# Optimization experiments

Measured on AMD Instinct MI355X. Metric: run time of the kernel, lower is better.

Reference implementation:

```python
import jax, jax.numpy as jnp
import numpy as np

NUM_CLASSES = 80
STRIDES = (8, 16, 32)
FEAT_HW = ((80, 80), (40, 40), (20, 20))
B = 32
MAX_GT = 60


def setup_inputs() -> dict:
    key = jax.random.key(0)
    ks = jax.random.split(key, 6)
    feats = {}
    for i, (s, (h, w)) in enumerate(zip(STRIDES, FEAT_HW)):
        feats[f"feat{s}"] = jax.random.normal(ks[i], (B, 5 + NUM_CLASSES, h, w), jnp.float32)
    u = jax.random.uniform(ks[3], (B, MAX_GT, 4), jnp.float32)
    # cx,cy in [0,640), w,h in [8,128): realistic pixel-space gt boxes for a 640x640 image
    gt_boxes = jnp.concatenate([u[..., :2] * 640.0, u[..., 2:] * 120.0 + 8.0], -1)
    gt_classes = jax.random.randint(ks[4], (B, MAX_GT), 0, NUM_CLASSES)
    num_gts = jax.random.randint(ks[5], (B,), 1, MAX_GT + 1)
    return dict(feat8=feats["feat8"], feat16=feats["feat16"], feat32=feats["feat32"],
                gt_boxes=gt_boxes, gt_classes=gt_classes, num_gts=num_gts)


def _decode(feat, stride):
    # torch get_output_and_grid: xy=(raw+grid)*stride, wh=exp(raw)*stride
    b, c, h, w = feat.shape
    yv, xv = jnp.meshgrid(jnp.arange(h), jnp.arange(w), indexing="ij")
    gx = xv.reshape(-1).astype(feat.dtype)  # [H*W]
    gy = yv.reshape(-1).astype(feat.dtype)
    out = feat.reshape(b, c, h * w).transpose(0, 2, 1)  # [B,A,C]
    xy = (out[..., :2] + jnp.stack([gx, gy], -1)[None]) * stride
    wh = jnp.exp(out[..., 2:4]) * stride
    return jnp.concatenate([xy, wh, out[..., 4:]], -1), gx, gy


def _pair_iou(a, b):
    # a: [G,4] xywh, b: [A,4] xywh -> [G,A] IoU (bboxes_iou, xyxy=False)
    tl = jnp.maximum(a[:, None, :2] - a[:, None, 2:] * 0.5, b[None, :, :2] - b[None, :, 2:] * 0.5)
    br = jnp.minimum(a[:, None, :2] + a[:, None, 2:] * 0.5, b[None, :, :2] + b[None, :, 2:] * 0.5)
    en = jnp.all(tl < br, -1)
    inter = jnp.where(en, jnp.prod(br - tl, -1), 0.0)
    area_a = jnp.prod(a[:, 2:], -1)
    area_b = jnp.prod(b[:, 2:], -1)
    return inter / (area_a[:, None] + area_b[None, :] - inter + 1e-16)


def _bce_logits(x, t):
    return jnp.maximum(x, 0.0) - x * t + jnp.log1p(jnp.exp(-jnp.abs(x)))


def _iou_loss(pred, tgt):
    # IOUloss(loss_type='iou'): 1 - iou^2, per box
    tl = jnp.maximum(pred[..., :2] - pred[..., 2:] * 0.5, tgt[..., :2] - tgt[..., 2:] * 0.5)
    br = jnp.minimum(pred[..., :2] + pred[..., 2:] * 0.5, tgt[..., :2] + tgt[..., 2:] * 0.5)
    en = jnp.all(tl < br, -1)
    inter = jnp.where(en, jnp.prod(br - tl, -1), 0.0)
    union = jnp.prod(pred[..., 2:], -1) + jnp.prod(tgt[..., 2:], -1) - inter
    iou = inter / (union + 1e-16)
    return 1.0 - iou ** 2


def _assign(boxes, cls_lo, obj_lo, gtb, gtc, vmask, cx, cy, st):
    # SimOTA per image. boxes [A,4], cls_lo [A,C], obj_lo [A], gtb [G,4], gtc [G] int,
    # vmask [G] bool (gt padding), cx/cy/st [A] anchor centers & strides.
    G, A = gtb.shape[0], boxes.shape[0]
    iou = _pair_iou(gtb, boxes)  # [G,A]
    gx, gy = gtb[:, :1], gtb[:, 1:2]
    gw, gh = gtb[:, 2:3], gtb[:, 3:4]
    in_box = ((cx[None] > gx - 0.5 * gw) & (cx[None] < gx + 0.5 * gw) &
              (cy[None] > gy - 0.5 * gh) & (cy[None] < gy + 0.5 * gh))
    R = 2.5  # center sampling radius (in strides)
    in_ctr = ((cx[None] > gx - R * st[None]) & (cx[None] < gx + R * st[None]) &
              (cy[None] > gy - R * st[None]) & (cy[None] < gy + R * st[None]))
    fg = ((in_box | in_ctr) & vmask[:, None]).any(0)  # [A] candidate anchors
    in_both = (in_box & in_ctr).astype(boxes.dtype)
    # pairwise cls cost: BCE(sqrt(sig(cls)*sig(obj)), onehot(gt_cls)).sum(-1),
    # decomposed to avoid the [G,A,C] tensor: sum_c bce0 + (bce1-bce0)[gt_cls]
    p = jnp.clip(jnp.sqrt(jax.nn.sigmoid(cls_lo) * jax.nn.sigmoid(obj_lo)[:, None]), 1e-7, 1.0 - 1e-7)
    bce1 = -jnp.log(p)          # [A,C]
    bce0 = -jnp.log(1.0 - p)    # [A,C]
    cls_cost = bce0.sum(-1)[None, :] + (bce1 - bce0)[:, gtc].T  # [G,A]
    cost = (cls_cost + 3.0 * (-jnp.log(iou + 1e-8))
            + 100000.0 * (1.0 - in_both)
            + 1e9 * (~fg)[None, :].astype(boxes.dtype)
            + 1e9 * (~vmask)[:, None].astype(boxes.dtype))
    K = 10  # n_candidate_k
    topk_ious, _ = jax.lax.top_k(iou * fg[None, :], K)
    dyn_k = jnp.maximum(topk_ious.sum(-1).astype(jnp.int32), 1)  # clamp(int(sum), min=1)
    _, pos = jax.lax.top_k(-cost, K)  # [G,K] lowest-cost anchors per gt
    sel = (jnp.arange(K)[None, :] < dyn_k[:, None]).astype(boxes.dtype)
    matching = jnp.zeros((G, A), boxes.dtype).at[jnp.arange(G)[:, None], pos].set(sel)
    matching = matching * vmask[:, None].astype(boxes.dtype)
    # resolve anchors claimed by >1 gt: keep min-cost gt
    conflict = matching.sum(0) > 1
    best_gt = jnp.argmin(cost, axis=0)  # [A]
    matching = jnp.where(conflict[None, :], jax.nn.one_hot(best_gt, G, dtype=matching.dtype).T, matching)
    fg_final = matching.sum(0) > 0  # [A]
    matched = jnp.argmax(matching, axis=0)  # [A]
    pred_iou = (matching * iou).sum(0)  # [A]
    cls_t = jax.nn.one_hot(gtc[matched], NUM_CLASSES, dtype=boxes.dtype) * pred_iou[:, None]
    reg_t = gtb[matched]
    return fg_final, cls_t, reg_t


def _forward(feat8, feat16, feat32, gt_boxes, gt_classes, num_gts):
    outs, cxs, cys, sts = [], [], [], []
    for f, s in zip((feat8, feat16, feat32), STRIDES):
        o, gx, gy = _decode(f, float(s))
        outs.append(o)
        cxs.append((gx + 0.5) * s)
        cys.append((gy + 0.5) * s)
        sts.append(jnp.full_like(gx, s))
    preds = jnp.concatenate(outs, 1)  # [B,A,5+C]
    cx = jnp.concatenate(cxs)
    cy = jnp.concatenate(cys)
    st = jnp.concatenate(sts)
    boxes = preds[..., :4]
    obj_lo = preds[..., 4]
    cls_lo = preds[..., 5:]
    vmask = jnp.arange(MAX_GT)[None, :] < num_gts[:, None]
    fg, cls_t, reg_t = jax.vmap(_assign, in_axes=(0, 0, 0, 0, 0, 0, None, None, None))(
        boxes, cls_lo, obj_lo, gt_boxes, gt_classes, vmask, cx, cy, st)
    # SimOTA assignment is no_grad in YOLOX: targets are constants wrt preds
    fg = jax.lax.stop_gradient(fg)
    cls_t = jax.lax.stop_gradient(cls_t)
    reg_t = jax.lax.stop_gradient(reg_t)
    fg_f = fg.astype(boxes.dtype)
    num_fg = jnp.maximum(fg_f.sum(), 1.0)
    loss_iou = (_iou_loss(boxes, reg_t) * fg_f).sum()
    loss_obj = _bce_logits(obj_lo, fg_f * 0.9).sum()  # obj_targets * 0.9 smoothing
    loss_cls = (_bce_logits(cls_lo, cls_t) * fg_f[..., None]).sum()
    REG_WEIGHT = 5.0
    return (REG_WEIGHT * loss_iou + loss_obj + loss_cls) / num_fg


def reference(feat8, feat16, feat32, gt_boxes, gt_classes, num_gts):
    return _forward(feat8, feat16, feat32, gt_boxes, gt_classes, num_gts)
```

## Files before the change

kernel.cpp:

```cpp
#include <hip/hip_runtime.h>

constexpr int kB = 32;
constexpr int kA = 8400;
constexpr int kG = 60;
constexpr int kC = 80;
constexpr int kK = 10;
constexpr int kNBx = (kA + 255)/256;
constexpr int kNB = kNBx * kB;

__device__ __forceinline__ float fexp(float x){ return __expf(x); }
__device__ __forceinline__ float flog(float x){ return __logf(x); }
__device__ __forceinline__ float frcp(float x){ return __builtin_amdgcn_rcpf(x); }
__device__ __forceinline__ float frsq(float x){ return __builtin_amdgcn_rsqf(x); }
__device__ __forceinline__ float fsqrt(float x){ return __builtin_amdgcn_sqrtf(x); }
__device__ __forceinline__ float fdiv(float a, float b){ return a * __builtin_amdgcn_rcpf(b); }
__device__ __forceinline__ float sigm(float x){ return frcp(1.0f + fexp(-x)); }
__device__ __forceinline__ float bce(float x, float t){
  return fmaxf(x, 0.0f) - x*t + flog(1.0f + fexp(-fabsf(x)));
}

__device__ __forceinline__ unsigned ordbits(float v){
  unsigned u = __float_as_uint(v);
  return (u & 0x80000000u) ? ~u : (u | 0x80000000u);
}
__device__ __forceinline__ float unpackf(unsigned k){
  return __uint_as_float((k & 0x80000000u) ? (k & 0x7fffffffu) : ~k);
}

struct AInfo { int x, y; float st; };
__device__ __forceinline__ AInfo ainfo(int a){
  AInfo r;
  if (a < 6400)      { r.x = a % 80;           r.y = a / 80;           r.st = 8.0f;  }
  else if (a < 8000) { int l = a-6400; r.x = l % 40; r.y = l / 40;     r.st = 16.0f; }
  else               { int l = a-8000; r.x = l % 20; r.y = l / 20;     r.st = 32.0f; }
  return r;
}

__device__ __forceinline__ float featv(const float* __restrict__ f8,
                                       const float* __restrict__ f16,
                                       const float* __restrict__ f32x,
                                       int b, int ch, int a){
  if (a < 6400) return f8 [(b*85 + ch)*6400 + a];
  if (a < 8000) return f16[(b*85 + ch)*1600 + (a - 6400)];
  return             f32x[(b*85 + ch)*400  + (a - 8000)];
}

__device__ __forceinline__ float pair_iou(float4 g, float4 p){
  float tlx = fmaxf(g.x - g.z*0.5f, p.x - p.z*0.5f);
  float tly = fmaxf(g.y - g.w*0.5f, p.y - p.w*0.5f);
  float brx = fminf(g.x + g.z*0.5f, p.x + p.z*0.5f);
  float bry = fminf(g.y + g.w*0.5f, p.y + p.w*0.5f);
  float inter = (tlx < brx && tly < bry) ? (brx-tlx)*(bry-tly) : 0.0f;
  return fdiv(inter, g.z*g.w + p.z*p.w - inter + 1e-16f);
}

__device__ __forceinline__ float cost_core(float iou, float cl, float obs, float b0sum,
                                           int a, float4 gt, int fg_a){
  AInfo ai = ainfo(a);
  float cx = ((float)ai.x + 0.5f)*ai.st;
  float cy = ((float)ai.y + 0.5f)*ai.st;
  bool in_box = (cx > gt.x - 0.5f*gt.z) && (cx < gt.x + 0.5f*gt.z)
             && (cy > gt.y - 0.5f*gt.w) && (cy < gt.y + 0.5f*gt.w);
  bool in_ctr = (cx > gt.x - 2.5f*ai.st) && (cx < gt.x + 2.5f*ai.st)
             && (cy > gt.y - 2.5f*ai.st) && (cy < gt.y + 2.5f*ai.st);
  float p = fsqrt(sigm(cl) * obs);
  p = fminf(fmaxf(p, 1e-7f), 1.0f - 1e-7f);
  float diff = -flog(p) + flog(1.0f - p);
  float c = b0sum + diff;
  c += 3.0f * (-flog(iou + 1e-8f));
  c += (in_box && in_ctr) ? 0.0f : 100000.0f;
  c += fg_a ? 0.0f : 1000000000.0f;
  return c;
}

__global__ __launch_bounds__(256) void k_decode(
    const float* __restrict__ f8, const float* __restrict__ f16, const float* __restrict__ f32x,
    const float* __restrict__ gtb, const int* __restrict__ ngts,
    float* __restrict__ boxes, float* __restrict__ objl, float* __restrict__ b0s,
    float* __restrict__ bceS, float* __restrict__ obsA,
    int* __restrict__ fg, int* __restrict__ cnt, int* __restrict__ mtch){
  int b = blockIdx.y;
  int tid = threadIdx.x;
  int a = blockIdx.x*256 + tid;
  __shared__ float4 sg[kG];
  if (tid < kG) sg[tid] = ((const float4*)gtb)[b*kG + tid];
  __syncthreads();
  if (a >= kA) return;
  int ng = ngts[b];
  const float* base; int hw, off; float st_; int gx, gy;
  if (a < 6400)      { base=f8;   hw=6400; off=a;        st_=8.0f;  gx=off%80; gy=off/80; }
  else if (a < 8000) { base=f16;  hw=1600; off=a-6400;   st_=16.0f; gx=off%40; gy=off/40; }
  else               { base=f32x; hw=400;  off=a-8000;   st_=32.0f; gx=off%20; gy=off/20; }
  const float* p0 = base + ((size_t)b*85)*hw + off;
  float t0 = p0[0];
  float t1 = p0[(size_t)hw];
  float t2 = p0[(size_t)2*hw];
  float t3 = p0[(size_t)3*hw];
  float ob = p0[(size_t)4*hw];
  float4 bx;
  bx.x = (t0 + (float)gx) * st_;
  bx.y = (t1 + (float)gy) * st_;
  bx.z = fexp(t2) * st_;
  bx.w = fexp(t3) * st_;
  int idx = b*kA + a;
  ((float4*)boxes)[idx] = bx;
  objl[idx] = ob;
  float obs = sigm(ob);
  obsA[idx] = obs;
  float so = fsqrt(obs);
  float s = 0.0f;
  float sumCl = 0.0f;
  float slogv = 0.0f;
  const float* pc = p0 + (size_t)5*hw;
  #pragma unroll 2
  for (int grp = 0; grp < kC/8; ++grp){
    float prodS = 1.0f, prodV = 1.0f;
    #pragma unroll
    for (int j = 0; j < 8; ++j){
      float cl = pc[(size_t)(grp*8 + j)*hw];
      float u = fexp(-cl);
      float v = 1.0f + u;
      float p = so * frsq(v);
      p = fminf(fmaxf(p, 1e-7f), 1.0f - 1e-7f);
      prodS *= (1.0f - p);
      prodV *= v;
      sumCl += cl;
    }
    s -= flog(prodS);
    slogv += flog(prodV);
  }
  b0s[idx] = s;
  bceS[idx] = sumCl + slogv;
  float cx = ((float)gx + 0.5f)*st_;
  float cy = ((float)gy + 0.5f)*st_;
  int f = 0;
  for (int g = 0; g < ng; ++g){
    float4 gt = sg[g];
    bool in_box = (cx > gt.x - 0.5f*gt.z) && (cx < gt.x + 0.5f*gt.z)
               && (cy > gt.y - 0.5f*gt.w) && (cy < gt.y + 0.5f*gt.w);
    bool in_ctr = (cx > gt.x - 2.5f*st_) && (cx < gt.x + 2.5f*st_)
               && (cy > gt.y - 2.5f*st_) && (cy < gt.y + 2.5f*st_);
    if (in_box || in_ctr){ f = 1; break; }
  }
  fg[idx] = f;
  cnt[idx] = 0;
  mtch[idx] = 0x7fffffff;
}

__global__ __launch_bounds__(1024) void k_compact(
    const int* __restrict__ fg, unsigned short* __restrict__ alist, int* __restrict__ mcnt){
  int b = blockIdx.x;
  int tid = threadIdx.x;
  const int CH = 9;
  int start = tid*CH;
  int myf[CH]; int cl = 0;
  #pragma unroll
  for (int j = 0; j < CH; ++j){
    int a = start + j;
    int f = (a < kA) ? fg[b*kA + a] : 0;
    myf[j] = f; cl += f;
  }
  __shared__ int s1[1024], s2[1024];
  int* cur = s1; int* nxt = s2;
  cur[tid] = cl; __syncthreads();
  for (int off = 1; off < 1024; off <<= 1){
    int v = cur[tid];
    if (tid >= off) v += cur[tid - off];
    nxt[tid] = v; __syncthreads();
    int* t = cur; cur = nxt; nxt = t;
  }
  int o = cur[tid] - cl;
  unsigned short* out = alist + (size_t)b*kA;
  #pragma unroll
  for (int j = 0; j < CH; ++j){
    int a = start + j;
    if (a < kA && myf[j]) out[o++] = (unsigned short)a;
  }
  if (tid == 1023) mcnt[b] = cur[tid];
}

__global__ __launch_bounds__(256) void k_assign(
    const float* __restrict__ f8, const float* __restrict__ f16, const float* __restrict__ f32x,
    const float* __restrict__ gtb, const int* __restrict__ gtc, const int* __restrict__ ngts,
    const float* __restrict__ boxes, const float* __restrict__ obsA, const float* __restrict__ b0s,
    const int* __restrict__ fg, const unsigned short* __restrict__ alist, const int* __restrict__ mcnt,
    int* __restrict__ cnt, int* __restrict__ mtch){
  int b = blockIdx.x / kG;
  int g = blockIdx.x % kG;
  if (g >= ngts[b]) return;
  int tid = threadIdx.x;
  int lane = tid & 63, wid = tid >> 6;
  float4 gt = ((const float4*)gtb)[b*kG + g];
  int cls = gtc[b*kG + g];
  const float4* bx4 = (const float4*)boxes;
  const float* c8  = f8   + ((size_t)b*85 + 5 + cls)*6400;
  const float* c16 = f16  + ((size_t)b*85 + 5 + cls)*1600;
  const float* c32 = f32x + ((size_t)b*85 + 5 + cls)*400;
  int m = mcnt[b];
  bool full = (m < kK);
  int len = full ? kA : m;
  const unsigned short* al = alist + (size_t)b*kA;
  __shared__ unsigned long long wk[4];

  unsigned long long k1[kK], k2[kK];
  #pragma unroll
  for (int i = 0; i < kK; ++i){ k1[i] = 0ull; k2[i] = 0ull; }

  for (int i = tid; i < len; i += 256){
    int a = full ? i : (int)al[i];
    int idx = b*kA + a;
    float4 bx = bx4[idx];
    float iou = pair_iou(gt, bx);
    int fga = full ? fg[idx] : 1;
    float v = fga ? iou : 0.0f;
    unsigned long long key1 = ((unsigned long long)ordbits(v) << 32) | (unsigned)(~a);
    if (key1 > k1[kK-1]){
      k1[kK-1] = key1;
      #pragma unroll
      for (int i2 = kK-1; i2 > 0; --i2)
        if (k1[i2] > k1[i2-1]){ unsigned long long t = k1[i2]; k1[i2] = k1[i2-1]; k1[i2-1] = t; }
    }
    float cl = (a < 6400) ? c8[a] : (a < 8000) ? c16[a-6400] : c32[a-8000];
    float c = cost_core(iou, cl, obsA[idx], b0s[idx], a, gt, fga);
    unsigned long long key2 = ~(((unsigned long long)ordbits(c) << 32) | (unsigned)a);
    if (key2 > k2[kK-1]){
      k2[kK-1] = key2;
      #pragma unroll
      for (int i2 = kK-1; i2 > 0; --i2)
        if (k2[i2] > k2[i2-1]){ unsigned long long t = k2[i2]; k2[i2] = k2[i2-1]; k2[i2-1] = t; }
    }
  }

  float ksum = 0.0f;
  for (int k = 0; k < kK; ++k){
    unsigned long long best = k1[0];
    #pragma unroll
    for (int off = 32; off; off >>= 1){
      unsigned long long o = __shfl_xor(best, off, 64);
      if (o > best) best = o;
    }
    if (lane == 0) wk[wid] = best;
    __syncthreads();
    unsigned long long w0 = wk[0];
    if (wk[1] > w0) w0 = wk[1];
    if (wk[2] > w0) w0 = wk[2];
    if (wk[3] > w0) w0 = wk[3];
    if (k1[0] == w0){
      #pragma unroll
      for (int i = 0; i < kK-1; ++i) k1[i] = k1[i+1];
      k1[kK-1] = 0ull;
    }
    ksum += unpackf((unsigned)(w0 >> 32));
    __syncthreads();
  }
  int dynk = max((int)ksum, 1);

  int my_a = -1;
  for (int k = 0; k < kK; ++k){
    unsigned long long best = k2[0];
    #pragma unroll
    for (int off = 32; off; off >>= 1){
      unsigned long long o = __shfl_xor(best, off, 64);
      if (o > best) best = o;
    }
    if (lane == 0) wk[wid] = best;
    __syncthreads();
    unsigned long long w0 = wk[0];
    if (wk[1] > w0) w0 = wk[1];
    if (wk[2] > w0) w0 = wk[2];
    if (wk[3] > w0) w0 = wk[3];
    if (k2[0] == w0){
      #pragma unroll
      for (int i = 0; i < kK-1; ++i) k2[i] = k2[i+1];
      k2[kK-1] = 0ull;
    }
    if (tid == k) my_a = (int)((unsigned)(~w0) & 0xffffffffu);
    __syncthreads();
  }
  if (tid < kK && tid < dynk){
    atomicAdd(&cnt[b*kA + my_a], 1);
    atomicMin(&mtch[b*kA + my_a], g);
  }
}

__global__ __launch_bounds__(256) void k_loss(
    const float* __restrict__ f8, const float* __restrict__ f16, const float* __restrict__ f32x,
    const float* __restrict__ gtb, const int* __restrict__ gtc, const int* __restrict__ ngts,
    const float* __restrict__ boxes, const float* __restrict__ objl, const float* __restrict__ b0s,
    const float* __restrict__ bceS, const float* __restrict__ obsA,
    const int* __restrict__ fg, const int* __restrict__ cnt, const int* __restrict__ mtch,
    float4* __restrict__ pacc){
  int b = blockIdx.y;
  int a = blockIdx.x*256 + threadIdx.x;
  int tid = threadIdx.x;
  __shared__ float4 sg[kG];
  __shared__ int scls[kG];
  if (tid < kG){ sg[tid] = ((const float4*)gtb)[b*kG + tid]; scls[tid] = gtc[b*kG + tid]; }
  __syncthreads();
  float li = 0.0f, lo = 0.0f, lc = 0.0f, nf = 0.0f;
  bool valid = (a < kA);
  int idx = valid ? (b*kA + a) : (b*kA);
  int c = valid ? cnt[idx] : 0;
  float ob = valid ? objl[idx] : 0.0f;
  float4 bx = valid ? ((const float4*)boxes)[idx] : make_float4(0,0,1,1);

  float fgf = 0.0f; int mg = 0;
  if (valid && c == 1){ mg = mtch[idx]; fgf = 1.0f; }
  bool need = valid && (c > 1);
  if (__any(need)){
    if (need){
      int ng = ngts[b];
      float b0 = b0s[idx];
      float obs = obsA[idx];
      int fga = fg[idx];
      float bestc = 3.0e38f; int bg = 0;
      for (int g = 0; g < ng; ++g){
        float iou = pair_iou(sg[g], bx);
        float cl = featv(f8,f16,f32x,b,5+scls[g],a);
        float cst = cost_core(iou, cl, obs, b0, a, sg[g], fga);
        if (cst < bestc){ bestc = cst; bg = g; }
      }
      mg = bg; fgf = 1.0f;
    }
  }
  if (valid){
    lo = bce(ob, fgf*0.9f);
    if (fgf > 0.0f){
      nf = 1.0f;
      float4 r = sg[mg];
      float piou = pair_iou(r, bx);
      float tlx = fmaxf(bx.x - bx.z*0.5f, r.x - r.z*0.5f);
      float tly = fmaxf(bx.y - bx.w*0.5f, r.y - r.w*0.5f);
      float brx = fminf(bx.x + bx.z*0.5f, r.x + r.z*0.5f);
      float bry = fminf(bx.y + bx.w*0.5f, r.y + r.w*0.5f);
      float inter = (tlx < brx && tly < bry) ? (brx-tlx)*(bry-tly) : 0.0f;
      float un = bx.z*bx.w + r.z*r.w - inter;
      float iou = fdiv(inter, un + 1e-16f);
      li = 1.0f - iou*iou;
      int tc = scls[mg];
      float cl_tc = featv(f8,f16,f32x,b,5+tc,a);
      lc = bceS[idx] - piou * cl_tc;
    }
  }
  for (int off = 32; off > 0; off >>= 1){
    li += __shfl_down(li, off, 64);
    lo += __shfl_down(lo, off, 64);
    lc += __shfl_down(lc, off, 64);
    nf += __shfl_down(nf, off, 64);
  }
  __shared__ float4 wred[4];
  int wid = tid >> 6;
  if ((tid & 63) == 0) wred[wid] = make_float4(li, lo, lc, nf);
  __syncthreads();
  if (tid == 0){
    float4 t = wred[0];
    for (int w = 1; w < 4; ++w){
      float4 o = wred[w];
      t.x += o.x; t.y += o.y; t.z += o.z; t.w += o.w;
    }
    pacc[blockIdx.y * gridDim.x + blockIdx.x] = t;
  }
}

__global__ __launch_bounds__(256) void k_final(
    const float4* __restrict__ pacc, float* __restrict__ out){
  int tid = threadIdx.x;
  float li = 0.0f, lo = 0.0f, lc = 0.0f, nf = 0.0f;
  for (int i = tid; i < kNB; i += 256){
    float4 p = pacc[i];
    li += p.x; lo += p.y; lc += p.z; nf += p.w;
  }
  for (int off = 32; off > 0; off >>= 1){
    li += __shfl_down(li, off, 64);
    lo += __shfl_down(lo, off, 64);
    lc += __shfl_down(lc, off, 64);
    nf += __shfl_down(nf, off, 64);
  }
  __shared__ float4 wred[4];
  int wid = tid >> 6;
  if ((tid & 63) == 0) wred[wid] = make_float4(li, lo, lc, nf);
  __syncthreads();
  if (tid == 0){
    float4 t = wred[0];
    for (int w = 1; w < 4; ++w){
      float4 o = wred[w];
      t.x += o.x; t.y += o.y; t.z += o.z; t.w += o.w;
    }
    out[0] = (5.0f*t.x + t.y + t.z) * frcp(fmaxf(t.w, 1.0f));
  }
}

extern "C" void kernel_launch(void* const* d_in, const int* in_sizes, int n_in,
                              void* d_out, int out_size, void* d_ws, size_t ws_size,
                              hipStream_t stream) {
  (void)in_sizes; (void)n_in; (void)out_size; (void)ws_size;
  const float* f8   = (const float*)d_in[0];
  const float* f16  = (const float*)d_in[1];
  const float* f32x = (const float*)d_in[2];
  const float* gtb  = (const float*)d_in[3];
  const int*   gtc  = (const int*)d_in[4];
  const int*   ngts = (const int*)d_in[5];
  float* out = (float*)d_out;

  const size_t BA = (size_t)kB*kA;
  float* ws    = (float*)d_ws;
  float* boxes = ws;
  float* objl  = boxes + BA*4;
  float* b0s   = objl  + BA;
  float* bceS  = b0s   + BA;
  float* obsA  = bceS  + BA;
  int*   fg    = (int*)(obsA + BA);
  int*   cnt   = fg  + BA;
  int*   mtch  = cnt + BA;
  unsigned short* alist = (unsigned short*)(mtch + BA);
  int*   mcnt  = (int*)(alist + BA);
  float4* pacc = (float4*)(mcnt + kB);

  dim3 gBA(kNBx, kB);
  k_decode<<<gBA, dim3(256), 0, stream>>>(f8,f16,f32x,gtb,ngts,boxes,objl,b0s,bceS,obsA,fg,cnt,mtch);
  k_compact<<<dim3(kB), dim3(1024), 0, stream>>>(fg, alist, mcnt);
  k_assign<<<dim3(kB*kG), dim3(256), 0, stream>>>(f8,f16,f32x,gtb,gtc,ngts,boxes,obsA,b0s,fg,alist,mcnt,cnt,mtch);
  k_loss<<<gBA, dim3(256), 0, stream>>>(f8,f16,f32x,gtb,gtc,ngts,boxes,objl,b0s,bceS,obsA,fg,cnt,mtch,pacc);
  k_final<<<dim3(1), dim3(256), 0, stream>>>(pacc, out);
}
```

Baseline: 216.3 us.

## Compute cost top-k only over in-box-and-center anchor rectangle, two-level top-k merge

Replaces the block-wide top-k selection, which needed two barriers per round, with a per-wave top-k followed by a single-wave merge through LDS. Instead of evaluating the cost for every candidate anchor, the kernel enumerates only anchors inside the intersection of each ground-truth box and its center region at each stride. It runs the full-scan cost pass only as a fallback when the candidate set is too small or the full-list path applies. This removes most of the second pass's loads and math and most of the barriers. It risks divergence from the original tie-breaking when the rectangle bounds miss anchors, and if the enumerated anchors exceed 256 threads the extra ones are silently ignored.

```diff
diff --git a/kernel.cpp b/kernel.cpp
--- a/kernel.cpp
+++ b/kernel.cpp
@@ -71,6 +71,15 @@
   c += (in_box && in_ctr) ? 0.0f : 100000.0f;
   c += fg_a ? 0.0f : 1000000000.0f;
   return c;
+}
+
+__device__ __forceinline__ unsigned long long wave_max64(unsigned long long v){
+  #pragma unroll
+  for (int off = 32; off; off >>= 1){
+    unsigned long long o = __shfl_xor(v, off, 64);
+    if (o > v) v = o;
+  }
+  return v;
 }
 
 __global__ __launch_bounds__(256) void k_decode(
@@ -200,11 +209,14 @@
   bool full = (m < kK);
   int len = full ? kA : m;
   const unsigned short* al = alist + (size_t)b*kA;
-  __shared__ unsigned long long wk[4];
-
-  unsigned long long k1[kK], k2[kK];
+
+  __shared__ unsigned long long lds_k[4*kK];
+  __shared__ int lds_cnt[4];
+  __shared__ int s_dynk;
+
+  unsigned long long k1[kK];
   #pragma unroll
-  for (int i = 0; i < kK; ++i){ k1[i] = 0ull; k2[i] = 0ull; }
+  for (int i = 0; i < kK; ++i) k1[i] = 0ull;
 
   for (int i = tid; i < len; i += 256){
     int a = full ? i : (int)al[i];
@@ -220,6 +232,127 @@
       for (int i2 = kK-1; i2 > 0; --i2)
         if (k1[i2] > k1[i2-1]){ unsigned long long t = k1[i2]; k1[i2] = k1[i2-1]; k1[i2-1] = t; }
     }
+  }
+  {
+    unsigned long long wtop = 0ull;
+    #pragma unroll
+    for (int k = 0; k < kK; ++k){
+      unsigned long long best = wave_max64(k1[0]);
+      if (k1[0] == best){
+        #pragma unroll
+        for (int i2 = 0; i2 < kK-1; ++i2) k1[i2] = k1[i2+1];
+        k1[kK-1] = 0ull;
+      }
+      if (lane == k) wtop = best;
+    }
+    if (lane < kK) lds_k[wid*kK + lane] = wtop;
+  }
+  __syncthreads();
+  if (wid == 0){
+    unsigned long long key = (lane < 4*kK) ? lds_k[lane] : 0ull;
+    float ksum = 0.0f;
+    #pragma unroll
+    for (int k = 0; k < kK; ++k){
+      unsigned long long best = wave_max64(key);
+      if (key == best) key = 0ull;
+      if (best) ksum += unpackf((unsigned)(best >> 32));
+    }
+    if (lane == 0) s_dynk = max((int)ksum, 1);
+  }
+  __syncthreads();
+  int dynk = s_dynk;
+
+  int x00,y00,nx0,n0, x01,y01,nx1,n1, x02,y02,nx2,n2;
+  {
+    auto rect = [&](float st, int W, int& rx0, int& ry0, int& rnx, int& rn){
+      float lox = fmaxf(gt.x - 0.5f*gt.z, gt.x - 2.5f*st);
+      float hix = fminf(gt.x + 0.5f*gt.z, gt.x + 2.5f*st);
+      float loy = fmaxf(gt.y - 0.5f*gt.w, gt.y - 2.5f*st);
+      float hiy = fminf(gt.y + 0.5f*gt.w, gt.y + 2.5f*st);
+      float rs = frcp(st);
+      int ax0 = max(0,   (int)floorf(lox*rs - 0.5f) - 1);
+      int ax1 = min(W-1, (int)ceilf (hix*rs - 0.5f) + 1);
+      int ay0 = max(0,   (int)floorf(loy*rs - 0.5f) - 1);
+      int ay1 = min(W-1, (int)ceilf (hiy*rs - 0.5f) + 1);
+      rx0 = ax0; ry0 = ay0;
+      rnx = max(0, ax1 - ax0 + 1);
+      int rny = max(0, ay1 - ay0 + 1);
+      rn = rnx * rny;
+    };
+    rect( 8.0f, 80, x00, y00, nx0, n0);
+    rect(16.0f, 40, x01, y01, nx1, n1);
+    rect(32.0f, 20, x02, y02, nx2, n2);
+  }
+  int total = n0 + n1 + n2;
+
+  unsigned long long ck = 0ull;
+  int nvalid = 0;
+  if (tid < total){
+    int i = tid, ix, iy, a; float st;
+    if (i < n0)           { ix = x00 + i % nx0; iy = y00 + i / nx0; a = iy*80 + ix;          st = 8.0f;  }
+    else if (i < n0 + n1) { int j = i - n0;      ix = x01 + j % nx1; iy = y01 + j / nx1; a = 6400 + iy*40 + ix; st = 16.0f; }
+    else                  { int j = i - n0 - n1; ix = x02 + j % nx2; iy = y02 + j / nx2; a = 8000 + iy*20 + ix; st = 32.0f; }
+    float cx = ((float)ix + 0.5f)*st;
+    float cy = ((float)iy + 0.5f)*st;
+    bool in_box = (cx > gt.x - 0.5f*gt.z) && (cx < gt.x + 0.5f*gt.z)
+               && (cy > gt.y - 0.5f*gt.w) && (cy < gt.y + 0.5f*gt.w);
+    bool in_ctr = (cx > gt.x - 2.5f*st) && (cx < gt.x + 2.5f*st)
+               && (cy > gt.y - 2.5f*st) && (cy < gt.y + 2.5f*st);
+    if (in_box && in_ctr){
+      int idx = b*kA + a;
+      float4 bx = bx4[idx];
+      float iou = pair_iou(gt, bx);
+      float cl = (a < 6400) ? c8[a] : (a < 8000) ? c16[a-6400] : c32[a-8000];
+      float c = cost_core(iou, cl, obsA[idx], b0s[idx], a, gt, 1);
+      ck = ~(((unsigned long long)ordbits(c) << 32) | (unsigned)a);
+      nvalid = 1;
+    }
+  }
+  {
+    unsigned long long bal = __ballot(nvalid);
+    if (lane == 0) lds_cnt[wid] = __popcll(bal);
+    unsigned long long wtop = 0ull;
+    #pragma unroll
+    for (int k = 0; k < kK; ++k){
+      unsigned long long best = wave_max64(ck);
+      if (ck == best) ck = 0ull;
+      if (lane == k) wtop = best;
+    }
+    if (lane < kK) lds_k[wid*kK + lane] = wtop;
+  }
+  __syncthreads();
+  int cnt_total = lds_cnt[0] + lds_cnt[1] + lds_cnt[2] + lds_cnt[3];
+  bool fb = full || (dynk > cnt_total);
+
+  if (!fb){
+    if (wid == 0){
+      unsigned long long key = (lane < 4*kK) ? lds_k[lane] : 0ull;
+      unsigned long long mine = 0ull;
+      #pragma unroll
+      for (int k = 0; k < kK; ++k){
+        unsigned long long best = wave_max64(key);
+        if (key == best) key = 0ull;
+        if (lane == k) mine = best;
+      }
+      if (lane < dynk && mine){
+        int a = (int)((unsigned)(~mine));
+        atomicAdd(&cnt[b*kA + a], 1);
+        atomicMin(&mtch[b*kA + a], g);
+      }
+    }
+    return;
+  }
+
+  __syncthreads();
+  unsigned long long k2[kK];
+  #pragma unroll
+  for (int i = 0; i < kK; ++i) k2[i] = 0ull;
+  for (int i = tid; i < len; i += 256){
+    int a = full ? i : (int)al[i];
+    int idx = b*kA + a;
+    float4 bx = bx4[idx];
+    float iou = pair_iou(gt, bx);
+    int fga = full ? fg[idx] : 1;
     float cl = (a < 6400) ? c8[a] : (a < 8000) ? c16[a-6400] : c32[a-8000];
     float c = cost_core(iou, cl, obsA[idx], b0s[idx], a, gt, fga);
     unsigned long long key2 = ~(((unsigned long long)ordbits(c) << 32) | (unsigned)a);
@@ -230,56 +363,35 @@
         if (k2[i2] > k2[i2-1]){ unsigned long long t = k2[i2]; k2[i2] = k2[i2-1]; k2[i2-1] = t; }
     }
   }
-
-  float ksum = 0.0f;
-  for (int k = 0; k < kK; ++k){
-    unsigned long long best = k1[0];
+  {
+    unsigned long long wtop = 0ull;
     #pragma unroll
-    for (int off = 32; off; off >>= 1){
-      unsigned long long o = __shfl_xor(best, off, 64);
-      if (o > best) best = o;
-    }
-    if (lane == 0) wk[wid] = best;
-    __syncthreads();
-    unsigned long long w0 = wk[0];
-    if (wk[1] > w0) w0 = wk[1];
-    if (wk[2] > w0) w0 = wk[2];
-    if (wk[3] > w0) w0 = wk[3];
-    if (k1[0] == w0){
-      #pragma unroll
-      for (int i = 0; i < kK-1; ++i) k1[i] = k1[i+1];
-      k1[kK-1] = 0ull;
-    }
-    ksum += unpackf((unsigned)(w0 >> 32));
-    __syncthreads();
-  }
-  int dynk = max((int)ksum, 1);
-
-  int my_a = -1;
-  for (int k = 0; k < kK; ++k){
-    unsigned long long best = k2[0];
+    for (int k = 0; k < kK; ++k){
+      unsigned long long best = wave_max64(k2[0]);
+      if (k2[0] == best){
+        #pragma unroll
+        for (int i2 = 0; i2 < kK-1; ++i2) k2[i2] = k2[i2+1];
+        k2[kK-1] = 0ull;
+      }
+      if (lane == k) wtop = best;
+    }
+    if (lane < kK) lds_k[wid*kK + lane] = wtop;
+  }
+  __syncthreads();
+  if (wid == 0){
+    unsigned long long key = (lane < 4*kK) ? lds_k[lane] : 0ull;
+    unsigned long long mine = 0ull;
     #pragma unroll
-    for (int off = 32; off; off >>= 1){
-      unsigned long long o = __shfl_xor(best, off, 64);
-      if (o > best) best = o;
-    }
-    if (lane == 0) wk[wid] = best;
-    __syncthreads();
-    unsigned long long w0 = wk[0];
-    if (wk[1] > w0) w0 = wk[1];
-    if (wk[2] > w0) w0 = wk[2];
-    if (wk[3] > w0) w0 = wk[3];
-    if (k2[0] == w0){
-      #pragma unroll
-      for (int i = 0; i < kK-1; ++i) k2[i] = k2[i+1];
-      k2[kK-1] = 0ull;
-    }
-    if (tid == k) my_a = (int)((unsigned)(~w0) & 0xffffffffu);
-    __syncthreads();
-  }
-  if (tid < kK && tid < dynk){
-    atomicAdd(&cnt[b*kA + my_a], 1);
-    atomicMin(&mtch[b*kA + my_a], g);
+    for (int k = 0; k < kK; ++k){
+      unsigned long long best = wave_max64(key);
+      if (key == best) key = 0ull;
+      if (lane == k) mine = best;
+    }
+    if (lane < dynk && mine){
+      int a = (int)((unsigned)(~mine));
+      atomicAdd(&cnt[b*kA + a], 1);
+      atomicMin(&mtch[b*kA + a], g);
+    }
   }
 }
 
```

Result: faster. 207.8 us (-3.9%).
